# Performance work log

Hardware: AMD Instinct MI355X
Metric: run time of the kernel (lower is better)

## Reference

```python
import jax, jax.numpy as jnp
import numpy as np

K = 2  # top-k experts per token


def setup_inputs() -> dict:
    key = jax.random.key(0)
    kx, kw = jax.random.split(key)
    x = jax.random.normal(kx, (4, 4096, 4096), dtype=jnp.float32)
    W = jax.random.normal(kw, (64, 4096), dtype=jnp.float32) * (4096 ** -0.5)
    return {"x": x, "W": W}


def reference(x, W):
    # gate: logits[b,s,e] = x[b,s,d] @ W[e,d]^T
    logits = jnp.einsum('bsd,ed->bse', x, W)
    scores, idx = jax.lax.top_k(logits, K)           # [B,S,K], [B,S,K]
    probs = jax.nn.softmax(scores, axis=-1)          # softmax over the k selected experts
    return probs, idx
```

## Files before the change

### kernel.cpp

```cpp
#include <hip/hip_runtime.h>
#include <math.h>


typedef float f32x4 __attribute__((ext_vector_type(4)));
typedef short bf16x8 __attribute__((ext_vector_type(8)));
typedef unsigned int u32;

#define NE 64
#define TOK 32
#define CK 128
#define THREADS 512
#define LDE 68

__device__ __forceinline__ u32 cvtpk(float lo, float hi) {
  u32 r;
  asm("v_cvt_pk_bf16_f32 %0, %1, %2" : "=v"(r) : "v"(lo), "v"(hi));
  return r;
}
__device__ __forceinline__ float asf(u32 u) {
  return __builtin_bit_cast(float, u);
}
__device__ __forceinline__ void cvt8(const f32x4 a, const f32x4 b,
                                     uint4& hp, uint4& lp) {
  hp.x = cvtpk(a.x, a.y);
  hp.y = cvtpk(a.z, a.w);
  hp.z = cvtpk(b.x, b.y);
  hp.w = cvtpk(b.z, b.w);
  lp.x = cvtpk(a.x - asf(hp.x << 16), a.y - asf(hp.x & 0xFFFF0000u));
  lp.y = cvtpk(a.z - asf(hp.y << 16), a.w - asf(hp.y & 0xFFFF0000u));
  lp.z = cvtpk(b.x - asf(hp.z << 16), b.y - asf(hp.z & 0xFFFF0000u));
  lp.w = cvtpk(b.z - asf(hp.w << 16), b.w - asf(hp.w & 0xFFFF0000u));
}
__device__ __forceinline__ void gload16(const void* gsrc, void* ldst) {
  __builtin_amdgcn_global_load_lds(
      (const __attribute__((address_space(1))) void*)gsrc,
      (__attribute__((address_space(3))) void*)ldst, 16, 0, 0);
}

__global__ __launch_bounds__(256)
void wprep(const float* __restrict__ Wg, uint2* __restrict__ Who,
           uint2* __restrict__ Wlo) {
  const int i = blockIdx.x * 256 + threadIdx.x;
  const f32x4 v = *((const f32x4*)Wg + i);
  uint2 hp, lp;
  hp.x = cvtpk(v.x, v.y);
  hp.y = cvtpk(v.z, v.w);
  lp.x = cvtpk(v.x - asf(hp.x << 16), v.y - asf(hp.x & 0xFFFF0000u));
  lp.y = cvtpk(v.z - asf(hp.y << 16), v.w - asf(hp.y & 0xFFFF0000u));
  Who[i] = hp;
  Wlo[i] = lp;
}

__global__ __launch_bounds__(THREADS, 2)
void gemm_topk(const float* __restrict__ x, const u32* __restrict__ Whg,
               const u32* __restrict__ Wlg, float* __restrict__ out_probs,
               float* __restrict__ out_idx, int D) {
  __shared__ __align__(16) char smem[49152];

  const int tid = threadIdx.x;
  const int w   = tid >> 6;
  const int l   = tid & 63;
  const int kw  = w & 3;
  const int eh  = w >> 2;
  const int m0  = blockIdx.x * TOK;
  const int nCh = D / CK;
  const int Du  = D / 2;

  const int g   = l >> 4;
  const int r16 = l & 15;

  const int rowA = 2 * w + (l >> 5);
  const int rowB = 16 + rowA;
  const int bA   = (l & 31) ^ (rowA & 7);
  const int bB   = (l & 31) ^ (rowB & 7);
  const float* gA = x + (size_t)(m0 + rowA) * D + bA * 4;
  const float* gB = x + (size_t)(m0 + rowB) * D + bB * 4;

  const u32* wh0 = Whg + (size_t)(eh * 32 + 0  + r16) * Du + kw * 16 + g * 4;
  const u32* wh1 = Whg + (size_t)(eh * 32 + 16 + r16) * Du + kw * 16 + g * 4;
  const u32* wl0 = Wlg + (size_t)(eh * 32 + 0  + r16) * Du + kw * 16 + g * 4;
  const u32* wl1 = Wlg + (size_t)(eh * 32 + 16 + r16) * Du + kw * 16 + g * 4;

  const int c0 = kw * 8 + g * 2;
  const int a00 = r16 * 512 + ((c0       ^ (r16 & 7)) << 4);
  const int a01 = r16 * 512 + (((c0 + 1) ^ (r16 & 7)) << 4);
  const int r1  = 16 + r16;
  const int a10 = r1 * 512 + ((c0       ^ (r1 & 7)) << 4);
  const int a11 = r1 * 512 + (((c0 + 1) ^ (r1 & 7)) << 4);

  f32x4 acc[2][2];
#pragma unroll
  for (int m = 0; m < 2; ++m)
#pragma unroll
    for (int n = 0; n < 2; ++n) acc[m][n] = (f32x4){0.f, 0.f, 0.f, 0.f};

  gload16(gA, smem + w * 1024);
  gload16(gB, smem + 8192 + w * 1024);
  if (nCh > 1) {
    gload16(gA + CK, smem + 16384 + w * 1024);
    gload16(gB + CK, smem + 16384 + 8192 + w * 1024);
  }
  asm volatile("s_waitcnt vmcnt(2)\n\ts_barrier" ::: "memory");

  for (int c = 0; c < nCh; ++c) {
    const int rb = (c % 3) * 16384;

    const size_t ko = (size_t)c * (CK / 2);
    const bf16x8 bh0 = *(const bf16x8*)(wh0 + ko);
    const bf16x8 bh1 = *(const bf16x8*)(wh1 + ko);
    const bf16x8 bl0 = *(const bf16x8*)(wl0 + ko);
    const bf16x8 bl1 = *(const bf16x8*)(wl1 + ko);

    if (c + 2 < nCh) {
      const int wb = ((c + 2) % 3) * 16384;
      gload16(gA + (size_t)(c + 2) * CK, smem + wb + w * 1024);
      gload16(gB + (size_t)(c + 2) * CK, smem + wb + 8192 + w * 1024);
    }

    const f32x4 t00 = *(const f32x4*)(smem + rb + a00);
    const f32x4 t01 = *(const f32x4*)(smem + rb + a01);
    const f32x4 t10 = *(const f32x4*)(smem + rb + a10);
    const f32x4 t11 = *(const f32x4*)(smem + rb + a11);
    uint4 hp0, lp0, hp1, lp1;
    cvt8(t00, t01, hp0, lp0);
    cvt8(t10, t11, hp1, lp1);
    const bf16x8 ah0 = __builtin_bit_cast(bf16x8, hp0);
    const bf16x8 al0 = __builtin_bit_cast(bf16x8, lp0);
    const bf16x8 ah1 = __builtin_bit_cast(bf16x8, hp1);
    const bf16x8 al1 = __builtin_bit_cast(bf16x8, lp1);

    acc[0][0] = __builtin_amdgcn_mfma_f32_16x16x32_bf16(ah0, bh0, acc[0][0], 0, 0, 0);
    acc[0][0] = __builtin_amdgcn_mfma_f32_16x16x32_bf16(ah0, bl0, acc[0][0], 0, 0, 0);
    acc[0][0] = __builtin_amdgcn_mfma_f32_16x16x32_bf16(al0, bh0, acc[0][0], 0, 0, 0);
    acc[0][1] = __builtin_amdgcn_mfma_f32_16x16x32_bf16(ah0, bh1, acc[0][1], 0, 0, 0);
    acc[0][1] = __builtin_amdgcn_mfma_f32_16x16x32_bf16(ah0, bl1, acc[0][1], 0, 0, 0);
    acc[0][1] = __builtin_amdgcn_mfma_f32_16x16x32_bf16(al0, bh1, acc[0][1], 0, 0, 0);
    acc[1][0] = __builtin_amdgcn_mfma_f32_16x16x32_bf16(ah1, bh0, acc[1][0], 0, 0, 0);
    acc[1][0] = __builtin_amdgcn_mfma_f32_16x16x32_bf16(ah1, bl0, acc[1][0], 0, 0, 0);
    acc[1][0] = __builtin_amdgcn_mfma_f32_16x16x32_bf16(al1, bh0, acc[1][0], 0, 0, 0);
    acc[1][1] = __builtin_amdgcn_mfma_f32_16x16x32_bf16(ah1, bh1, acc[1][1], 0, 0, 0);
    acc[1][1] = __builtin_amdgcn_mfma_f32_16x16x32_bf16(ah1, bl1, acc[1][1], 0, 0, 0);
    acc[1][1] = __builtin_amdgcn_mfma_f32_16x16x32_bf16(al1, bh1, acc[1][1], 0, 0, 0);

    asm volatile("s_barrier" ::: "memory");
  }

  __syncthreads();

  float* R = (float*)smem;
#pragma unroll
  for (int m = 0; m < 2; ++m)
#pragma unroll
    for (int n = 0; n < 2; ++n)
#pragma unroll
      for (int r = 0; r < 4; ++r)
        R[w * 1024 + ((m * 2 + n) * 4 + r) * 64 + l] = acc[m][n][r];
  __syncthreads();

  float vals[4];
  int dsti[4];
#pragma unroll
  for (int i = 0; i < 4; ++i) {
    const int j = tid + i * THREADS;
    const int t = j >> 6, e = j & 63;
    const int mm = t >> 4, nn = (e >> 4) & 1, ee = e >> 5;
    const int rr = t & 3;
    const int ll = ((t & 15) >> 2) * 16 + (e & 15);
    float v = 0.f;
#pragma unroll
    for (int k = 0; k < 4; ++k)
      v += R[(ee * 4 + k) * 1024 + ((mm * 2 + nn) * 4 + rr) * 64 + ll];
    vals[i] = v;
    dsti[i] = t * LDE + e;
  }
  __syncthreads();
  float* Lf = (float*)smem;
#pragma unroll
  for (int i = 0; i < 4; ++i) Lf[dsti[i]] = vals[i];
  __syncthreads();

  if (tid < TOK) {
    const float* row = &Lf[tid * LDE];
    float b0 = -INFINITY, b1 = -INFINITY;
    int i0 = 0, i1 = 0;
#pragma unroll
    for (int e = 0; e < NE; ++e) {
      const float val = row[e];
      if (val > b0) { b1 = b0; i1 = i0; b0 = val; i0 = e; }
      else if (val > b1) { b1 = val; i1 = e; }
    }
    const float e1  = expf(b1 - b0);
    const float inv = 1.f / (1.f + e1);
    const int tok = m0 + tid;
    out_probs[tok * 2 + 0] = inv;
    out_probs[tok * 2 + 1] = e1 * inv;
    out_idx[tok * 2 + 0] = (float)i0;
    out_idx[tok * 2 + 1] = (float)i1;
  }
}

#define FEW 8
#define FCK 64
#define FLDT 68
#define FTOK 64
__global__ __launch_bounds__(512, 2)
void router_fused(const float* __restrict__ x, const float* __restrict__ W,
                  float* __restrict__ out_probs, float* __restrict__ out_idx,
                  int D) {
  __shared__ float As[2][FTOK][FLDT];
  const int tid = threadIdx.x;
  const int w = __builtin_amdgcn_readfirstlane(tid >> 6);
  const int lane = tid & 63;
  const int m0 = blockIdx.x * FTOK;
  const int nCh = D / FCK;
  const float* xrow = x + (size_t)(m0 + lane) * D;
  const float* __restrict__ wbase = W + (size_t)(w * FEW) * D;
  float acc[FEW];
#pragma unroll
  for (int e = 0; e < FEW; ++e) acc[e] = 0.f;
  {
    const f32x4 a = *reinterpret_cast<const f32x4*>(xrow + 4 * w);
    const f32x4 b = *reinterpret_cast<const f32x4*>(xrow + 4 * (w + 8));
    *reinterpret_cast<f32x4*>(&As[0][lane][4 * w]) = a;
    *reinterpret_cast<f32x4*>(&As[0][lane][4 * (w + 8)]) = b;
  }
  __syncthreads();
  for (int c = 0; c < nCh; ++c) {
    const int buf = c & 1;
    f32x4 na, nb;
    const bool more = (c + 1 < nCh);
    if (more) {
      const float* xn = xrow + (size_t)(c + 1) * FCK;
      na = *reinterpret_cast<const f32x4*>(xn + 4 * w);
      nb = *reinterpret_cast<const f32x4*>(xn + 4 * (w + 8));
    }
    const float* __restrict__ wp = wbase + (size_t)c * FCK;
#pragma unroll 2
    for (int kk = 0; kk < FCK / 4; ++kk) {
      const f32x4 xvv = *reinterpret_cast<const f32x4*>(&As[buf][lane][kk * 4]);
#pragma unroll
      for (int e = 0; e < FEW; ++e) {
        const f32x4 wv = *reinterpret_cast<const f32x4*>(wp + (size_t)e * D + kk * 4);
        acc[e] = fmaf(xvv.x, wv.x, acc[e]);
        acc[e] = fmaf(xvv.y, wv.y, acc[e]);
        acc[e] = fmaf(xvv.z, wv.z, acc[e]);
        acc[e] = fmaf(xvv.w, wv.w, acc[e]);
      }
    }
    __syncthreads();
    if (more) {
      *reinterpret_cast<f32x4*>(&As[buf ^ 1][lane][4 * w]) = na;
      *reinterpret_cast<f32x4*>(&As[buf ^ 1][lane][4 * (w + 8)]) = nb;
    }
    __syncthreads();
  }
  float* L = &As[0][0][0];
  *reinterpret_cast<f32x4*>(&L[lane * FLDT + w * FEW + 0]) =
      (f32x4){acc[0], acc[1], acc[2], acc[3]};
  *reinterpret_cast<f32x4*>(&L[lane * FLDT + w * FEW + 4]) =
      (f32x4){acc[4], acc[5], acc[6], acc[7]};
  __syncthreads();
  if (tid < FTOK) {
    const float* row = &L[tid * FLDT];
    float b0 = -INFINITY, b1 = -INFINITY;
    int i0 = 0, i1 = 0;
#pragma unroll
    for (int e = 0; e < NE; ++e) {
      const float val = row[e];
      if (val > b0) { b1 = b0; i1 = i0; b0 = val; i0 = e; }
      else if (val > b1) { b1 = val; i1 = e; }
    }
    const float e1 = expf(b1 - b0);
    const float inv = 1.f / (1.f + e1);
    const int tok = m0 + tid;
    out_probs[tok * 2 + 0] = inv;
    out_probs[tok * 2 + 1] = e1 * inv;
    out_idx[tok * 2 + 0] = (float)i0;
    out_idx[tok * 2 + 1] = (float)i1;
  }
}

extern "C" void kernel_launch(void* const* d_in, const int* in_sizes, int n_in,
                              void* d_out, int out_size, void* d_ws, size_t ws_size,
                              hipStream_t stream) {
  const float* x = (const float*)d_in[0];
  const float* W = (const float*)d_in[1];

  const int E = 64;
  const int D = in_sizes[1] / E;
  const int nTok = in_sizes[0] / D;

  float* probs = (float*)d_out;
  float* idxo  = (float*)d_out + (size_t)nTok * 2;

  const size_t wBytes = (size_t)E * D * sizeof(short);
  if (ws_size >= 2 * wBytes) {
    u32* Wh = (u32*)d_ws;
    u32* Wl = (u32*)((char*)d_ws + wBytes);
    hipLaunchKernelGGL(wprep, dim3((E * D / 4) / 256), dim3(256), 0, stream,
                       W, (uint2*)Wh, (uint2*)Wl);
    hipLaunchKernelGGL(gemm_topk, dim3(nTok / TOK), dim3(THREADS), 0, stream,
                       x, Wh, Wl, probs, idxo, D);
  } else {
    hipLaunchKernelGGL(router_fused, dim3(nTok / FTOK), dim3(512), 0, stream,
                       x, W, probs, idxo, D);
  }
}
```

Measured before the change: 85.14 us.

## Double token tile per block to reuse W fragments across 64 tokens

Raises the tokens per block from 32 to 64, so each wave computes four M-subtiles instead of two while loading the same W hi/lo fragments once per chunk. This halves global W traffic per token and the number of blocks. In exchange the triple-buffered LDS ring grows to 96KB, so only one block fits per CU despite launch_bounds(…,2), and register pressure rises from the 8 accumulators and 8 A fragments.

```diff
diff --git a/kernel.cpp b/kernel.cpp
--- a/kernel.cpp
+++ b/kernel.cpp
@@ -7,7 +7,7 @@
 typedef unsigned int u32;
 
 #define NE 64
-#define TOK 32
+#define TOK 64
 #define CK 128
 #define THREADS 512
 #define LDE 68
@@ -55,7 +55,7 @@
 void gemm_topk(const float* __restrict__ x, const u32* __restrict__ Whg,
                const u32* __restrict__ Wlg, float* __restrict__ out_probs,
                float* __restrict__ out_idx, int D) {
-  __shared__ __align__(16) char smem[49152];
+  __shared__ __align__(16) char smem[98304];
 
   const int tid = threadIdx.x;
   const int w   = tid >> 6;
@@ -69,12 +69,10 @@
   const int g   = l >> 4;
   const int r16 = l & 15;
 
-  const int rowA = 2 * w + (l >> 5);
-  const int rowB = 16 + rowA;
-  const int bA   = (l & 31) ^ (rowA & 7);
-  const int bB   = (l & 31) ^ (rowB & 7);
-  const float* gA = x + (size_t)(m0 + rowA) * D + bA * 4;
-  const float* gB = x + (size_t)(m0 + rowB) * D + bB * 4;
+  const int rbase = 2 * w + (l >> 5);
+  const int bsw   = (l & 31) ^ (rbase & 7);
+  const float* gX = x + (size_t)(m0 + rbase) * D + bsw * 4;
+  const size_t jstep = (size_t)16 * D;
 
   const u32* wh0 = Whg + (size_t)(eh * 32 + 0  + r16) * Du + kw * 16 + g * 4;
   const u32* wh1 = Whg + (size_t)(eh * 32 + 16 + r16) * Du + kw * 16 + g * 4;
@@ -82,28 +80,30 @@
   const u32* wl1 = Wlg + (size_t)(eh * 32 + 16 + r16) * Du + kw * 16 + g * 4;
 
   const int c0 = kw * 8 + g * 2;
-  const int a00 = r16 * 512 + ((c0       ^ (r16 & 7)) << 4);
-  const int a01 = r16 * 512 + (((c0 + 1) ^ (r16 & 7)) << 4);
-  const int r1  = 16 + r16;
-  const int a10 = r1 * 512 + ((c0       ^ (r1 & 7)) << 4);
-  const int a11 = r1 * 512 + (((c0 + 1) ^ (r1 & 7)) << 4);
-
-  f32x4 acc[2][2];
-#pragma unroll
-  for (int m = 0; m < 2; ++m)
+  int aoff[4][2];
+#pragma unroll
+  for (int m = 0; m < 4; ++m) {
+    const int row = m * 16 + r16;
+    aoff[m][0] = row * 512 + ((c0       ^ (r16 & 7)) << 4);
+    aoff[m][1] = row * 512 + (((c0 + 1) ^ (r16 & 7)) << 4);
+  }
+
+  f32x4 acc[4][2];
+#pragma unroll
+  for (int m = 0; m < 4; ++m)
 #pragma unroll
     for (int n = 0; n < 2; ++n) acc[m][n] = (f32x4){0.f, 0.f, 0.f, 0.f};
 
-  gload16(gA, smem + w * 1024);
-  gload16(gB, smem + 8192 + w * 1024);
-  if (nCh > 1) {
-    gload16(gA + CK, smem + 16384 + w * 1024);
-    gload16(gB + CK, smem + 16384 + 8192 + w * 1024);
-  }
-  asm volatile("s_waitcnt vmcnt(2)\n\ts_barrier" ::: "memory");
+#pragma unroll
+  for (int j = 0; j < 4; ++j)
+    gload16(gX + jstep * j, smem + j * 8192 + w * 1024);
+#pragma unroll
+  for (int j = 0; j < 4; ++j)
+    gload16(gX + jstep * j + CK, smem + 32768 + j * 8192 + w * 1024);
+  asm volatile("s_waitcnt vmcnt(4)\n\ts_barrier" ::: "memory");
 
   for (int c = 0; c < nCh; ++c) {
-    const int rb = (c % 3) * 16384;
+    const int rb = (c % 3) * 32768;
 
     const size_t ko = (size_t)c * (CK / 2);
     const bf16x8 bh0 = *(const bf16x8*)(wh0 + ko);
@@ -112,35 +112,32 @@
     const bf16x8 bl1 = *(const bf16x8*)(wl1 + ko);
 
     if (c + 2 < nCh) {
-      const int wb = ((c + 2) % 3) * 16384;
-      gload16(gA + (size_t)(c + 2) * CK, smem + wb + w * 1024);
-      gload16(gB + (size_t)(c + 2) * CK, smem + wb + 8192 + w * 1024);
-    }
-
-    const f32x4 t00 = *(const f32x4*)(smem + rb + a00);
-    const f32x4 t01 = *(const f32x4*)(smem + rb + a01);
-    const f32x4 t10 = *(const f32x4*)(smem + rb + a10);
-    const f32x4 t11 = *(const f32x4*)(smem + rb + a11);
-    uint4 hp0, lp0, hp1, lp1;
-    cvt8(t00, t01, hp0, lp0);
-    cvt8(t10, t11, hp1, lp1);
-    const bf16x8 ah0 = __builtin_bit_cast(bf16x8, hp0);
-    const bf16x8 al0 = __builtin_bit_cast(bf16x8, lp0);
-    const bf16x8 ah1 = __builtin_bit_cast(bf16x8, hp1);
-    const bf16x8 al1 = __builtin_bit_cast(bf16x8, lp1);
-
-    acc[0][0] = __builtin_amdgcn_mfma_f32_16x16x32_bf16(ah0, bh0, acc[0][0], 0, 0, 0);
-    acc[0][0] = __builtin_amdgcn_mfma_f32_16x16x32_bf16(ah0, bl0, acc[0][0], 0, 0, 0);
-    acc[0][0] = __builtin_amdgcn_mfma_f32_16x16x32_bf16(al0, bh0, acc[0][0], 0, 0, 0);
-    acc[0][1] = __builtin_amdgcn_mfma_f32_16x16x32_bf16(ah0, bh1, acc[0][1], 0, 0, 0);
-    acc[0][1] = __builtin_amdgcn_mfma_f32_16x16x32_bf16(ah0, bl1, acc[0][1], 0, 0, 0);
-    acc[0][1] = __builtin_amdgcn_mfma_f32_16x16x32_bf16(al0, bh1, acc[0][1], 0, 0, 0);
-    acc[1][0] = __builtin_amdgcn_mfma_f32_16x16x32_bf16(ah1, bh0, acc[1][0], 0, 0, 0);
-    acc[1][0] = __builtin_amdgcn_mfma_f32_16x16x32_bf16(ah1, bl0, acc[1][0], 0, 0, 0);
-    acc[1][0] = __builtin_amdgcn_mfma_f32_16x16x32_bf16(al1, bh0, acc[1][0], 0, 0, 0);
-    acc[1][1] = __builtin_amdgcn_mfma_f32_16x16x32_bf16(ah1, bh1, acc[1][1], 0, 0, 0);
-    acc[1][1] = __builtin_amdgcn_mfma_f32_16x16x32_bf16(ah1, bl1, acc[1][1], 0, 0, 0);
-    acc[1][1] = __builtin_amdgcn_mfma_f32_16x16x32_bf16(al1, bh1, acc[1][1], 0, 0, 0);
+      const int wb = ((c + 2) % 3) * 32768;
+      const size_t co = (size_t)(c + 2) * CK;
+#pragma unroll
+      for (int j = 0; j < 4; ++j)
+        gload16(gX + co + jstep * j, smem + wb + j * 8192 + w * 1024);
+    }
+
+    bf16x8 ah[4], al[4];
+#pragma unroll
+    for (int m = 0; m < 4; ++m) {
+      const f32x4 t0 = *(const f32x4*)(smem + rb + aoff[m][0]);
+      const f32x4 t1 = *(const f32x4*)(smem + rb + aoff[m][1]);
+      uint4 hp, lp;
+      cvt8(t0, t1, hp, lp);
+      ah[m] = __builtin_bit_cast(bf16x8, hp);
+      al[m] = __builtin_bit_cast(bf16x8, lp);
+    }
+#pragma unroll
+    for (int m = 0; m < 4; ++m) {
+      acc[m][0] = __builtin_amdgcn_mfma_f32_16x16x32_bf16(ah[m], bh0, acc[m][0], 0, 0, 0);
+      acc[m][0] = __builtin_amdgcn_mfma_f32_16x16x32_bf16(ah[m], bl0, acc[m][0], 0, 0, 0);
+      acc[m][0] = __builtin_amdgcn_mfma_f32_16x16x32_bf16(al[m], bh0, acc[m][0], 0, 0, 0);
+      acc[m][1] = __builtin_amdgcn_mfma_f32_16x16x32_bf16(ah[m], bh1, acc[m][1], 0, 0, 0);
+      acc[m][1] = __builtin_amdgcn_mfma_f32_16x16x32_bf16(ah[m], bl1, acc[m][1], 0, 0, 0);
+      acc[m][1] = __builtin_amdgcn_mfma_f32_16x16x32_bf16(al[m], bh1, acc[m][1], 0, 0, 0);
+    }
 
     asm volatile("s_barrier" ::: "memory");
   }
@@ -149,18 +146,18 @@
 
   float* R = (float*)smem;
 #pragma unroll
-  for (int m = 0; m < 2; ++m)
+  for (int m = 0; m < 4; ++m)
 #pragma unroll
     for (int n = 0; n < 2; ++n)
 #pragma unroll
       for (int r = 0; r < 4; ++r)
-        R[w * 1024 + ((m * 2 + n) * 4 + r) * 64 + l] = acc[m][n][r];
-  __syncthreads();
-
-  float vals[4];
-  int dsti[4];
-#pragma unroll
-  for (int i = 0; i < 4; ++i) {
+        R[w * 2048 + ((m * 2 + n) * 4 + r) * 64 + l] = acc[m][n][r];
+  __syncthreads();
+
+  float vals[8];
+  int dsti[8];
+#pragma unroll
+  for (int i = 0; i < 8; ++i) {
     const int j = tid + i * THREADS;
     const int t = j >> 6, e = j & 63;
     const int mm = t >> 4, nn = (e >> 4) & 1, ee = e >> 5;
@@ -169,14 +166,14 @@
     float v = 0.f;
 #pragma unroll
     for (int k = 0; k < 4; ++k)
-      v += R[(ee * 4 + k) * 1024 + ((mm * 2 + nn) * 4 + rr) * 64 + ll];
+      v += R[(ee * 4 + k) * 2048 + ((mm * 2 + nn) * 4 + rr) * 64 + ll];
     vals[i] = v;
     dsti[i] = t * LDE + e;
   }
   __syncthreads();
   float* Lf = (float*)smem;
 #pragma unroll
-  for (int i = 0; i < 4; ++i) Lf[dsti[i]] = vals[i];
+  for (int i = 0; i < 8; ++i) Lf[dsti[i]] = vals[i];
   __syncthreads();
 
   if (tid < TOK) {
```

Measured after the change: 75.96 us. 10.8% less time.
